# Kernel tuning notes

Measured on AMD Instinct MI355X. Metric: run time of the kernel, lower is better.

Reference implementation:

```python
import jax, jax.numpy as jnp
import numpy as np

EPS = 0.1        # entropic regularization
MAX_ITER = 50    # fixed iteration count (torch early-stops on host; we run all iters)
P = 1            # cost exponent
N_POINTS = 4096
D_FEAT = 2


def _cost_matrix(x, y):
    # x: [N, D], y: [M, D] -> C: [N, M], sum_d |x_i - y_j|^p
    return jnp.sum(jnp.abs(x[:, None, :] - y[None, :, :]) ** P, axis=-1)


def setup_inputs() -> dict:
    key = jax.random.key(0)
    k1, k2 = jax.random.split(key)
    x = jax.random.normal(k1, (N_POINTS, D_FEAT), dtype=jnp.float32)
    y = jax.random.normal(k2, (N_POINTS, D_FEAT), dtype=jnp.float32)
    return {"x": x, "y": y}


def reference(x, y):
    n, m = x.shape[0], y.shape[0]
    C = _cost_matrix(x, y)  # [N, M]
    log_mu = jnp.log(jnp.full((n,), 1.0 / n, dtype=x.dtype) + 1e-8)
    log_nu = jnp.log(jnp.full((m,), 1.0 / m, dtype=y.dtype) + 1e-8)

    def M(u, v):
        # modified cost: (-C + u_i + v_j) / eps
        return (-C + u[:, None] + v[None, :]) / EPS

    def step(carry, _):
        u, v = carry
        u = EPS * (log_mu - jax.scipy.special.logsumexp(M(u, v), axis=-1)) + u
        v = EPS * (log_nu - jax.scipy.special.logsumexp(M(u, v), axis=-2)) + v
        return (u, v), None

    u0 = jnp.zeros((n,), dtype=x.dtype)
    v0 = jnp.zeros((m,), dtype=y.dtype)
    (u, v), _ = jax.lax.scan(step, (u0, v0), None, length=MAX_ITER)

    pi = jnp.exp(M(u, v))                 # transport plan [N, M]
    cost = jnp.sum(pi * C)                # scalar (reduction='none', 2D input)
    return cost ** (1.0 / P), pi, C
```

## Files before the change

### kernel.cpp

```cpp
#include <hip/hip_runtime.h>


#define NPTS    4096
#define EPS_F   0.1f
#define S_L2E   14.426950408889634f
#define INV_SL  0.0693147180559945f
#define A_LOGMU (-0.8317725207f)
#define N_ITER  50
#define NLEAF   16
#define BSTRIDE 64
#define BAR_INTS ((NLEAF + 1 + NLEAF) * BSTRIDE)

typedef float f4u __attribute__((ext_vector_type(4), aligned(4)));

__device__ __forceinline__ float fexp2(float x) {
#if __has_builtin(__builtin_amdgcn_exp2f)
  return __builtin_amdgcn_exp2f(x);
#else
  float r;
  asm("v_exp_f32 %0, %1" : "=v"(r) : "v"(x));
  return r;
#endif
}

__device__ __forceinline__ float coh_load(const float* p) {
  return __hip_atomic_load(p, __ATOMIC_RELAXED, __HIP_MEMORY_SCOPE_AGENT);
}
__device__ __forceinline__ void coh_store(float* p, float x) {
  __hip_atomic_store(p, x, __ATOMIC_RELAXED, __HIP_MEMORY_SCOPE_AGENT);
}

__device__ __forceinline__ float wave_sum64(float x) {
#pragma unroll
  for (int off = 32; off > 0; off >>= 1) x += __shfl_xor(x, off, 64);
  return x;
}

__device__ __forceinline__ void grid_barrier(int* bar, int k, int arrpl) {
  __syncthreads();
  if (threadIdx.x == 0) {
    const int myleaf = blockIdx.x & (NLEAF - 1);
    const int old = __hip_atomic_fetch_add(bar + myleaf * BSTRIDE, 1,
                                           __ATOMIC_RELAXED,
                                           __HIP_MEMORY_SCOPE_AGENT);
    if (old == arrpl * k - 1)
      __hip_atomic_store(bar + (NLEAF + 1 + myleaf) * BSTRIDE, k,
                         __ATOMIC_RELAXED, __HIP_MEMORY_SCOPE_AGENT);
    for (;;) {
      int mn = k;
#pragma unroll
      for (int rr = 0; rr < NLEAF; ++rr) {
        const int f = __hip_atomic_load(bar + (NLEAF + 1 + rr) * BSTRIDE,
                                        __ATOMIC_RELAXED,
                                        __HIP_MEMORY_SCOPE_AGENT);
        mn = min(mn, f);
      }
      if (mn >= k) break;
      __builtin_amdgcn_s_sleep(1);
    }
  }
  __syncthreads();
}

#define QBLK  512
#define QTPB  1024
#define QARR  (QBLK / NLEAF)
#define QC    1024

__device__ __forceinline__ void stageWq(const float* __restrict__ part,
                                        float* __restrict__ sW, int tid,
                                        int colbase, bool zero) {
  float w = 0.f;
  if (!zero) {
    const int g = colbase + tid;
    const float s = ((coh_load(part + g) + coh_load(part + NPTS + g)) +
                     coh_load(part + 2 * NPTS + g)) +
                    coh_load(part + 3 * NPTS + g);
    w = (A_LOGMU - INV_SL * __log2f(s)) * S_L2E;
  }
  sW[tid] = w;
  __syncthreads();
}

__device__ __forceinline__ void phaseq(
    const float rx0, const float ry0, const float rx1, const float ry1,
    const float* __restrict__ sW, const float* __restrict__ sC0,
    const float* __restrict__ sC1, float* __restrict__ pout, int q, int row0,
    int lane) {
  float acc0 = 0.f, acc1 = 0.f;
#pragma unroll
  for (int jt = 0; jt < 4; ++jt) {
    const int j = lane * 4 + jt * 256;
    const float4 W  = *(const float4*)(sW + j);
    const float4 C0 = *(const float4*)(sC0 + j);
    const float4 C1 = *(const float4*)(sC1 + j);
    {
      const float a0 = (W.x - fabsf(rx0 - C0.x)) - fabsf(ry0 - C1.x);
      const float a1 = (W.y - fabsf(rx0 - C0.y)) - fabsf(ry0 - C1.y);
      const float a2 = (W.z - fabsf(rx0 - C0.z)) - fabsf(ry0 - C1.z);
      const float a3 = (W.w - fabsf(rx0 - C0.w)) - fabsf(ry0 - C1.w);
      acc0 += (fexp2(a0) + fexp2(a1)) + (fexp2(a2) + fexp2(a3));
    }
    {
      const float a0 = (W.x - fabsf(rx1 - C0.x)) - fabsf(ry1 - C1.x);
      const float a1 = (W.y - fabsf(rx1 - C0.y)) - fabsf(ry1 - C1.y);
      const float a2 = (W.z - fabsf(rx1 - C0.z)) - fabsf(ry1 - C1.z);
      const float a3 = (W.w - fabsf(rx1 - C0.w)) - fabsf(ry1 - C1.w);
      acc1 += (fexp2(a0) + fexp2(a1)) + (fexp2(a2) + fexp2(a3));
    }
  }
  const float S0 = wave_sum64(acc0);
  const float S1 = wave_sum64(acc1);
  if (lane == 0) {
    coh_store(pout + q * NPTS + row0, S0);
    coh_store(pout + q * NPTS + row0 + 1, S1);
  }
}

__global__ void __launch_bounds__(QTPB, 8)
sinkhorn_quarter(const float* __restrict__ x, const float* __restrict__ y,
                 float* __restrict__ pu, float* __restrict__ pv,
                 float* __restrict__ out, int* __restrict__ bar) {
  __shared__ float sW[QC];
  __shared__ float sC0u[QC], sC1u[QC];
  __shared__ float sC0v[QC], sC1v[QC];
  __shared__ float sCost[16];

  const int tid  = threadIdx.x;
  const int wv   = tid >> 6;
  const int lane = tid & 63;
  const int q    = blockIdx.x & 3;
  const int rg   = blockIdx.x >> 2;
  const int row0 = rg * 32 + wv * 2;
  const int colbase = q * QC;

  float rxu[2], ryu[2], rxv[2], ryv[2];
#pragma unroll
  for (int r = 0; r < 2; ++r) {
    const float2 xr = ((const float2*)x)[row0 + r];
    const float2 yr = ((const float2*)y)[row0 + r];
    rxu[r] = xr.x * S_L2E;  ryu[r] = xr.y * S_L2E;
    rxv[r] = yr.x * S_L2E;  ryv[r] = yr.y * S_L2E;
  }

  {
    const int g = colbase + tid;
    const float2 yc = ((const float2*)y)[g];
    const float2 xc = ((const float2*)x)[g];
    sC0u[tid] = yc.x * S_L2E;  sC1u[tid] = yc.y * S_L2E;
    sC0v[tid] = xc.x * S_L2E;  sC1v[tid] = xc.y * S_L2E;
  }
  __syncthreads();

  int k = 0;
  for (int it = 0; it < N_ITER; ++it) {
    stageWq(pv, sW, tid, colbase, it == 0);
    phaseq(rxu[0], ryu[0], rxu[1], ryu[1], sW, sC0u, sC1u, pu, q, row0, lane);
    grid_barrier(bar, ++k, QARR);
    stageWq(pu, sW, tid, colbase, false);
    phaseq(rxv[0], ryv[0], rxv[1], ryv[1], sW, sC0v, sC1v, pv, q, row0, lane);
    grid_barrier(bar, ++k, QARR);
  }
  stageWq(pv, sW, tid, colbase, false);

  float* __restrict__ pi = out + 1;
  float* __restrict__ cm = out + 1 + (size_t)NPTS * NPTS;
  float uu[2];
#pragma unroll
  for (int r = 0; r < 2; ++r) {
    const int g = row0 + r;
    const float su = ((coh_load(pu + g) + coh_load(pu + NPTS + g)) +
                      coh_load(pu + 2 * NPTS + g)) +
                     coh_load(pu + 3 * NPTS + g);
    uu[r] = (A_LOGMU - INV_SL * __log2f(su)) * S_L2E;
  }

  float costacc = 0.f;
#pragma unroll
  for (int jt = 0; jt < 4; ++jt) {
    const int j = lane * 4 + jt * 256;
    const float4 W  = *(const float4*)(sW + j);
    const float4 C0 = *(const float4*)(sC0u + j);
    const float4 C1 = *(const float4*)(sC1u + j);
#pragma unroll
    for (int r = 0; r < 2; ++r) {
      const float s0 = fabsf(rxu[r] - C0.x) + fabsf(ryu[r] - C1.x);
      const float s1 = fabsf(rxu[r] - C0.y) + fabsf(ryu[r] - C1.y);
      const float s2 = fabsf(rxu[r] - C0.z) + fabsf(ryu[r] - C1.z);
      const float s3 = fabsf(rxu[r] - C0.w) + fabsf(ryu[r] - C1.w);
      const float p0 = fexp2((uu[r] + W.x) - s0);
      const float p1 = fexp2((uu[r] + W.y) - s1);
      const float p2 = fexp2((uu[r] + W.z) - s2);
      const float p3 = fexp2((uu[r] + W.w) - s3);
      costacc = fmaf(p0, s0, costacc);
      costacc = fmaf(p1, s1, costacc);
      costacc = fmaf(p2, s2, costacc);
      costacc = fmaf(p3, s3, costacc);
      const size_t off = (size_t)(row0 + r) * NPTS + colbase + j;
      f4u pvv; pvv.x = p0; pvv.y = p1; pvv.z = p2; pvv.w = p3;
      f4u cv;  cv.x = s0 * INV_SL; cv.y = s1 * INV_SL;
      cv.z = s2 * INV_SL; cv.w = s3 * INV_SL;
      *(f4u*)(pi + off) = pvv;
      *(f4u*)(cm + off) = cv;
    }
  }
  const float cw = wave_sum64(costacc);
  if (lane == 0) sCost[wv] = cw;
  __syncthreads();
  if (tid == 0) {
    float c = 0.f;
#pragma unroll
    for (int w = 0; w < 16; ++w) c += sCost[w];
    atomicAdd(out, c * INV_SL);
  }
}

#define FBLK  256
#define FTPB  1024
#define WPB   (FTPB / 64)
#define RPW   2
#define HALFC 2048
#define NJT   (HALFC / 256)
#define FARR  (FBLK / NLEAF)

__device__ __forceinline__ void fb_stageW(const float* __restrict__ win,
                                          float* __restrict__ sW, int tid) {
  const int c = tid * 4;
  const float w0 = coh_load(win + c + 0), w1 = coh_load(win + c + 1);
  const float w2 = coh_load(win + c + 2), w3 = coh_load(win + c + 3);
  float4 W;
  W.x = w0 * S_L2E;  W.y = w1 * S_L2E;  W.z = w2 * S_L2E;  W.w = w3 * S_L2E;
  *(float4*)(sW + c) = W;
  __syncthreads();
}

__device__ __forceinline__ void fb_stageCoords(const float* __restrict__ colp,
                                               float* __restrict__ sC0,
                                               float* __restrict__ sC1,
                                               int tid) {
  const int c = tid * 4;
  const float4 a = ((const float4*)colp)[(c >> 1) + 0];
  const float4 b = ((const float4*)colp)[(c >> 1) + 1];
  float4 C0, C1;
  C0.x = a.x * S_L2E; C0.y = a.z * S_L2E; C0.z = b.x * S_L2E; C0.w = b.z * S_L2E;
  C1.x = a.y * S_L2E; C1.y = a.w * S_L2E; C1.z = b.y * S_L2E; C1.w = b.w * S_L2E;
  *(float4*)(sC0 + c) = C0;
  *(float4*)(sC1 + c) = C1;
}

__device__ __forceinline__ void fb_phase(const float* __restrict__ rx,
                                         const float* __restrict__ ry,
                                         const float* __restrict__ sW,
                                         const float* __restrict__ sC0,
                                         const float* __restrict__ sC1,
                                         float (*sPart)[RPW],
                                         float* __restrict__ wout,
                                         int row0blk, int wv, int lane,
                                         int tid, int base) {
  float acc0 = 0.f, acc1 = 0.f;
#pragma unroll
  for (int jt = 0; jt < NJT; ++jt) {
    const int j = base + jt * 256;
    const float4 W  = *(const float4*)(sW + j);
    const float4 C0 = *(const float4*)(sC0 + j);
    const float4 C1 = *(const float4*)(sC1 + j);
    {
      const float a0 = (W.x - fabsf(rx[0] - C0.x)) - fabsf(ry[0] - C1.x);
      const float a1 = (W.y - fabsf(rx[0] - C0.y)) - fabsf(ry[0] - C1.y);
      const float a2 = (W.z - fabsf(rx[0] - C0.z)) - fabsf(ry[0] - C1.z);
      const float a3 = (W.w - fabsf(rx[0] - C0.w)) - fabsf(ry[0] - C1.w);
      acc0 += (fexp2(a0) + fexp2(a1)) + (fexp2(a2) + fexp2(a3));
    }
    {
      const float a0 = (W.x - fabsf(rx[1] - C0.x)) - fabsf(ry[1] - C1.x);
      const float a1 = (W.y - fabsf(rx[1] - C0.y)) - fabsf(ry[1] - C1.y);
      const float a2 = (W.z - fabsf(rx[1] - C0.z)) - fabsf(ry[1] - C1.z);
      const float a3 = (W.w - fabsf(rx[1] - C0.w)) - fabsf(ry[1] - C1.w);
      acc1 += (fexp2(a0) + fexp2(a1)) + (fexp2(a2) + fexp2(a3));
    }
  }
  const float S0 = wave_sum64(acc0);
  const float S1 = wave_sum64(acc1);
  if (lane == 0) { sPart[wv][0] = S0; sPart[wv][1] = S1; }
  __syncthreads();
  if (tid < 16) {
    const int p = tid >> 1, r = tid & 1;
    const float S = sPart[2 * p][r] + sPart[2 * p + 1][r];
    coh_store(wout + row0blk + p * RPW + r, A_LOGMU - EPS_F * __logf(S));
  }
}

__global__ void __launch_bounds__(FTPB, 4)
sinkhorn_fallback(const float* __restrict__ x, const float* __restrict__ y,
                  float* __restrict__ u, float* __restrict__ v,
                  float* __restrict__ out, int* __restrict__ bar) {
  __shared__ float sW[NPTS];
  __shared__ float sC0y[NPTS], sC1y[NPTS];
  __shared__ float sC0x[NPTS], sC1x[NPTS];
  __shared__ float sPart[WPB][RPW];
  __shared__ float sCost[WPB];

  const int tid  = threadIdx.x;
  const int wv   = tid >> 6;
  const int lane = tid & 63;
  const int row0blk = blockIdx.x * (WPB / 2) * RPW;
  const int row0 = row0blk + (wv >> 1) * RPW;
  const int base = (wv & 1) * HALFC + lane * 4;

  float rxu[RPW], ryu[RPW], rxv[RPW], ryv[RPW];
#pragma unroll
  for (int r = 0; r < RPW; ++r) {
    const float2 xr = ((const float2*)x)[row0 + r];
    const float2 yr = ((const float2*)y)[row0 + r];
    rxu[r] = xr.x * S_L2E;  ryu[r] = xr.y * S_L2E;
    rxv[r] = yr.x * S_L2E;  ryv[r] = yr.y * S_L2E;
  }

  fb_stageCoords(y, sC0y, sC1y, tid);
  fb_stageCoords(x, sC0x, sC1x, tid);
  __syncthreads();

  int k = 0;
  for (int it = 0; it < N_ITER; ++it) {
    fb_stageW(v, sW, tid);
    fb_phase(rxu, ryu, sW, sC0y, sC1y, sPart, u, row0blk, wv, lane, tid, base);
    grid_barrier(bar, ++k, FARR);
    fb_stageW(u, sW, tid);
    fb_phase(rxv, ryv, sW, sC0x, sC1x, sPart, v, row0blk, wv, lane, tid, base);
    grid_barrier(bar, ++k, FARR);
  }
  fb_stageW(v, sW, tid);

  float* __restrict__ pi = out + 1;
  float* __restrict__ cm = out + 1 + (size_t)NPTS * NPTS;
  float uu[RPW];
#pragma unroll
  for (int r = 0; r < RPW; ++r) uu[r] = coh_load(u + row0 + r) * S_L2E;

  float costacc = 0.f;
#pragma unroll 2
  for (int jt = 0; jt < NJT; ++jt) {
    const int j = base + jt * 256;
    const float4 W  = *(const float4*)(sW + j);
    const float4 C0 = *(const float4*)(sC0y + j);
    const float4 C1 = *(const float4*)(sC1y + j);
#pragma unroll
    for (int r = 0; r < RPW; ++r) {
      const float s0 = fabsf(rxu[r] - C0.x) + fabsf(ryu[r] - C1.x);
      const float s1 = fabsf(rxu[r] - C0.y) + fabsf(ryu[r] - C1.y);
      const float s2 = fabsf(rxu[r] - C0.z) + fabsf(ryu[r] - C1.z);
      const float s3 = fabsf(rxu[r] - C0.w) + fabsf(ryu[r] - C1.w);
      const float p0 = fexp2((uu[r] + W.x) - s0);
      const float p1 = fexp2((uu[r] + W.y) - s1);
      const float p2 = fexp2((uu[r] + W.z) - s2);
      const float p3 = fexp2((uu[r] + W.w) - s3);
      costacc = fmaf(p0, s0, costacc);
      costacc = fmaf(p1, s1, costacc);
      costacc = fmaf(p2, s2, costacc);
      costacc = fmaf(p3, s3, costacc);
      const size_t off = (size_t)(row0 + r) * NPTS + j;
      f4u pvv; pvv.x = p0; pvv.y = p1; pvv.z = p2; pvv.w = p3;
      f4u cv;  cv.x = s0 * INV_SL; cv.y = s1 * INV_SL;
      cv.z = s2 * INV_SL; cv.w = s3 * INV_SL;
      *(f4u*)(pi + off) = pvv;
      *(f4u*)(cm + off) = cv;
    }
  }
  const float cw = wave_sum64(costacc);
  if (lane == 0) sCost[wv] = cw;
  __syncthreads();
  if (tid == 0) {
    float c = 0.f;
#pragma unroll
    for (int w = 0; w < WPB; ++w) c += sCost[w];
    atomicAdd(out, c * INV_SL);
  }
}

__global__ void sinkhorn_init(float* __restrict__ buf, int* __restrict__ bar,
                              float* __restrict__ out) {
  const int i = blockIdx.x * blockDim.x + threadIdx.x;
  if (i < 8 * NPTS) coh_store(buf + i, 0.f);
  if (i < BAR_INTS)
    __hip_atomic_store(bar + i, 0, __ATOMIC_RELAXED, __HIP_MEMORY_SCOPE_AGENT);
  if (i == 0) out[0] = 0.f;
}

extern "C" void kernel_launch(void* const* d_in, const int* in_sizes, int n_in,
                              void* d_out, int out_size, void* d_ws,
                              size_t ws_size, hipStream_t stream) {
  const float* x = (const float*)d_in[0];
  const float* y = (const float*)d_in[1];
  float* pu = (float*)d_ws;
  float* pv = pu + 4 * NPTS;
  int* bar = (int*)(pv + 4 * NPTS);
  float* out = (float*)d_out;

  sinkhorn_init<<<dim3(128), dim3(256), 0, stream>>>(pu, bar, out);

  int maxb = 0;
  hipOccupancyMaxActiveBlocksPerMultiprocessor(&maxb, sinkhorn_quarter, QTPB,
                                               0);

  if (maxb >= 2) {
    void* args[6];
    args[0] = (void*)&x;  args[1] = (void*)&y;
    args[2] = (void*)&pu; args[3] = (void*)&pv;
    args[4] = (void*)&out; args[5] = (void*)&bar;
    hipLaunchCooperativeKernel((void*)sinkhorn_quarter, dim3(QBLK), dim3(QTPB),
                               args, 0, stream);
  } else {
    float* u = pu;
    float* v = pv;
    void* args[6];
    args[0] = (void*)&x;  args[1] = (void*)&y;
    args[2] = (void*)&u;  args[3] = (void*)&v;
    args[4] = (void*)&out; args[5] = (void*)&bar;
    hipLaunchCooperativeKernel((void*)sinkhorn_fallback, dim3(FBLK),
                               dim3(FTPB), args, 0, stream);
  }
}
```

Measured before the change: 716.4 us.

## Replace grid barriers with per-block dependency flags and double-buffered partials

Removes the two full grid barriers per Sinkhorn iteration. Each block now publishes a per-block completion flag and waits only on the 128 producer blocks whose partial sums feed its column quarter. The u/v partial-sum buffers are double-buffered by iteration parity, so fast blocks can run ahead without overwriting data that slower blocks still need. This trades a global sync for many more flag polls per block (128 threads spinning), which adds memory traffic to the flag lines.

Measured after the change: 708.5 us. No clear change (-1.1%).

```diff
diff --git a/kernel.cpp b/kernel.cpp
--- a/kernel.cpp
+++ b/kernel.cpp
@@ -29,6 +29,12 @@
 __device__ __forceinline__ void coh_store(float* p, float x) {
   __hip_atomic_store(p, x, __ATOMIC_RELAXED, __HIP_MEMORY_SCOPE_AGENT);
 }
+__device__ __forceinline__ int coh_load_i(const int* p) {
+  return __hip_atomic_load(p, __ATOMIC_RELAXED, __HIP_MEMORY_SCOPE_AGENT);
+}
+__device__ __forceinline__ void coh_store_i(int* p, int x) {
+  __hip_atomic_store(p, x, __ATOMIC_RELAXED, __HIP_MEMORY_SCOPE_AGENT);
+}
 
 __device__ __forceinline__ float wave_sum64(float x) {
 #pragma unroll
@@ -36,50 +42,20 @@
   return x;
 }
 
-__device__ __forceinline__ void grid_barrier(int* bar, int k, int arrpl) {
-  __syncthreads();
-  if (threadIdx.x == 0) {
-    const int myleaf = blockIdx.x & (NLEAF - 1);
-    const int old = __hip_atomic_fetch_add(bar + myleaf * BSTRIDE, 1,
-                                           __ATOMIC_RELAXED,
-                                           __HIP_MEMORY_SCOPE_AGENT);
-    if (old == arrpl * k - 1)
-      __hip_atomic_store(bar + (NLEAF + 1 + myleaf) * BSTRIDE, k,
-                         __ATOMIC_RELAXED, __HIP_MEMORY_SCOPE_AGENT);
-    for (;;) {
-      int mn = k;
-#pragma unroll
-      for (int rr = 0; rr < NLEAF; ++rr) {
-        const int f = __hip_atomic_load(bar + (NLEAF + 1 + rr) * BSTRIDE,
-                                        __ATOMIC_RELAXED,
-                                        __HIP_MEMORY_SCOPE_AGENT);
-        mn = min(mn, f);
-      }
-      if (mn >= k) break;
-      __builtin_amdgcn_s_sleep(1);
-    }
-  }
-  __syncthreads();
-}
-
 #define QBLK  512
 #define QTPB  1024
-#define QARR  (QBLK / NLEAF)
 #define QC    1024
-
-__device__ __forceinline__ void stageWq(const float* __restrict__ part,
-                                        float* __restrict__ sW, int tid,
-                                        int colbase, bool zero) {
-  float w = 0.f;
-  if (!zero) {
-    const int g = colbase + tid;
-    const float s = ((coh_load(part + g) + coh_load(part + NPTS + g)) +
-                     coh_load(part + 2 * NPTS + g)) +
-                    coh_load(part + 3 * NPTS + g);
-    w = (A_LOGMU - INV_SL * __log2f(s)) * S_L2E;
-  }
-  sW[tid] = w;
-  __syncthreads();
+#define FSTR  32
+#define PLANE (4 * NPTS)
+
+__device__ __forceinline__ void stage_from(const float* __restrict__ P,
+                                           float* __restrict__ sW, int tid,
+                                           int colbase) {
+  const int g = colbase + tid;
+  const float s = ((coh_load(P + g) + coh_load(P + NPTS + g)) +
+                   coh_load(P + 2 * NPTS + g)) +
+                  coh_load(P + 3 * NPTS + g);
+  sW[tid] = (A_LOGMU - INV_SL * __log2f(s)) * S_L2E;
 }
 
 __device__ __forceinline__ void phaseq(
@@ -118,9 +94,10 @@
 }
 
 __global__ void __launch_bounds__(QTPB, 8)
-sinkhorn_quarter(const float* __restrict__ x, const float* __restrict__ y,
-                 float* __restrict__ pu, float* __restrict__ pv,
-                 float* __restrict__ out, int* __restrict__ bar) {
+sinkhorn_flags(const float* __restrict__ x, const float* __restrict__ y,
+               float* __restrict__ pu, float* __restrict__ pv,
+               int* __restrict__ uflg, int* __restrict__ vflg,
+               float* __restrict__ out) {
   __shared__ float sW[QC];
   __shared__ float sC0u[QC], sC1u[QC];
   __shared__ float sC0v[QC], sC1v[QC];
@@ -133,6 +110,8 @@
   const int rg   = blockIdx.x >> 2;
   const int row0 = rg * 32 + wv * 2;
   const int colbase = q * QC;
+  const int b = blockIdx.x;
+  const int pbase = q * 128;
 
   float rxu[2], ryu[2], rxv[2], ryv[2];
 #pragma unroll
@@ -142,7 +121,6 @@
     rxu[r] = xr.x * S_L2E;  ryu[r] = xr.y * S_L2E;
     rxv[r] = yr.x * S_L2E;  ryv[r] = yr.y * S_L2E;
   }
-
   {
     const int g = colbase + tid;
     const float2 yc = ((const float2*)y)[g];
@@ -152,26 +130,53 @@
   }
   __syncthreads();
 
-  int k = 0;
   for (int it = 0; it < N_ITER; ++it) {
-    stageWq(pv, sW, tid, colbase, it == 0);
-    phaseq(rxu[0], ryu[0], rxu[1], ryu[1], sW, sC0u, sC1u, pu, q, row0, lane);
-    grid_barrier(bar, ++k, QARR);
-    stageWq(pu, sW, tid, colbase, false);
-    phaseq(rxv[0], ryv[0], rxv[1], ryv[1], sW, sC0v, sC1v, pv, q, row0, lane);
-    grid_barrier(bar, ++k, QARR);
-  }
-  stageWq(pv, sW, tid, colbase, false);
+    if (it > 0 && tid < 128)
+      while (coh_load_i(vflg + (pbase + tid) * FSTR) < it)
+        __builtin_amdgcn_s_sleep(1);
+    __syncthreads();
+    if (it > 0)
+      stage_from(pv + ((it - 1) & 1) * PLANE, sW, tid, colbase);
+    else
+      sW[tid] = 0.f;
+    __syncthreads();
+    phaseq(rxu[0], ryu[0], rxu[1], ryu[1], sW, sC0u, sC1u,
+           pu + (it & 1) * PLANE, q, row0, lane);
+    __syncthreads();
+    if (tid == 0) coh_store_i(uflg + b * FSTR, it + 1);
+
+    if (tid < 128)
+      while (coh_load_i(uflg + (pbase + tid) * FSTR) < it + 1)
+        __builtin_amdgcn_s_sleep(1);
+    __syncthreads();
+    stage_from(pu + (it & 1) * PLANE, sW, tid, colbase);
+    __syncthreads();
+    phaseq(rxv[0], ryv[0], rxv[1], ryv[1], sW, sC0v, sC1v,
+           pv + (it & 1) * PLANE, q, row0, lane);
+    __syncthreads();
+    if (tid == 0) coh_store_i(vflg + b * FSTR, it + 1);
+  }
+
+  if (tid < 128)
+    while (coh_load_i(vflg + (pbase + tid) * FSTR) < N_ITER)
+      __builtin_amdgcn_s_sleep(1);
+  else if (tid < 132)
+    while (coh_load_i(uflg + (rg * 4 + (tid - 128)) * FSTR) < N_ITER)
+      __builtin_amdgcn_s_sleep(1);
+  __syncthreads();
+  stage_from(pv + ((N_ITER - 1) & 1) * PLANE, sW, tid, colbase);
+  __syncthreads();
 
   float* __restrict__ pi = out + 1;
   float* __restrict__ cm = out + 1 + (size_t)NPTS * NPTS;
+  const float* __restrict__ PU = pu + ((N_ITER - 1) & 1) * PLANE;
   float uu[2];
 #pragma unroll
   for (int r = 0; r < 2; ++r) {
     const int g = row0 + r;
-    const float su = ((coh_load(pu + g) + coh_load(pu + NPTS + g)) +
-                      coh_load(pu + 2 * NPTS + g)) +
-                     coh_load(pu + 3 * NPTS + g);
+    const float su = ((coh_load(PU + g) + coh_load(PU + NPTS + g)) +
+                      coh_load(PU + 2 * NPTS + g)) +
+                     coh_load(PU + 3 * NPTS + g);
     uu[r] = (A_LOGMU - INV_SL * __log2f(su)) * S_L2E;
   }
 
@@ -223,6 +228,32 @@
 #define NJT   (HALFC / 256)
 #define FARR  (FBLK / NLEAF)
 
+__device__ __forceinline__ void grid_barrier(int* bar, int k, int arrpl) {
+  __syncthreads();
+  if (threadIdx.x == 0) {
+    const int myleaf = blockIdx.x & (NLEAF - 1);
+    const int old = __hip_atomic_fetch_add(bar + myleaf * BSTRIDE, 1,
+                                           __ATOMIC_RELAXED,
+                                           __HIP_MEMORY_SCOPE_AGENT);
+    if (old == arrpl * k - 1)
+      __hip_atomic_store(bar + (NLEAF + 1 + myleaf) * BSTRIDE, k,
+                         __ATOMIC_RELAXED, __HIP_MEMORY_SCOPE_AGENT);
+    for (;;) {
+      int mn = k;
+#pragma unroll
+      for (int rr = 0; rr < NLEAF; ++rr) {
+        const int f = __hip_atomic_load(bar + (NLEAF + 1 + rr) * BSTRIDE,
+                                        __ATOMIC_RELAXED,
+                                        __HIP_MEMORY_SCOPE_AGENT);
+        mn = min(mn, f);
+      }
+      if (mn >= k) break;
+      __builtin_amdgcn_s_sleep(1);
+    }
+  }
+  __syncthreads();
+}
+
 __device__ __forceinline__ void fb_stageW(const float* __restrict__ win,
                                           float* __restrict__ sW, int tid) {
   const int c = tid * 4;
@@ -377,10 +408,17 @@
   }
 }
 
-__global__ void sinkhorn_init(float* __restrict__ buf, int* __restrict__ bar,
+#define NFLG (QBLK * FSTR)
+
+__global__ void sinkhorn_init(float* __restrict__ planes,
+                              int* __restrict__ flags,
+                              int* __restrict__ bar,
                               float* __restrict__ out) {
   const int i = blockIdx.x * blockDim.x + threadIdx.x;
-  if (i < 8 * NPTS) coh_store(buf + i, 0.f);
+  if (i < 4 * PLANE) coh_store(planes + i, 0.f);
+  if (i < 2 * NFLG)
+    __hip_atomic_store(flags + i, 0, __ATOMIC_RELAXED,
+                       __HIP_MEMORY_SCOPE_AGENT);
   if (i < BAR_INTS)
     __hip_atomic_store(bar + i, 0, __ATOMIC_RELAXED, __HIP_MEMORY_SCOPE_AGENT);
   if (i == 0) out[0] = 0.f;
@@ -392,26 +430,28 @@
   const float* x = (const float*)d_in[0];
   const float* y = (const float*)d_in[1];
   float* pu = (float*)d_ws;
-  float* pv = pu + 4 * NPTS;
-  int* bar = (int*)(pv + 4 * NPTS);
+  float* pv = pu + 2 * PLANE;
+  int* uflg = (int*)(pv + 2 * PLANE);
+  int* vflg = uflg + NFLG;
+  int* bar  = vflg + NFLG;
   float* out = (float*)d_out;
 
-  sinkhorn_init<<<dim3(128), dim3(256), 0, stream>>>(pu, bar, out);
+  sinkhorn_init<<<dim3(256), dim3(256), 0, stream>>>(pu, uflg, bar, out);
 
   int maxb = 0;
-  hipOccupancyMaxActiveBlocksPerMultiprocessor(&maxb, sinkhorn_quarter, QTPB,
-                                               0);
+  hipOccupancyMaxActiveBlocksPerMultiprocessor(&maxb, sinkhorn_flags, QTPB, 0);
 
   if (maxb >= 2) {
-    void* args[6];
-    args[0] = (void*)&x;  args[1] = (void*)&y;
-    args[2] = (void*)&pu; args[3] = (void*)&pv;
-    args[4] = (void*)&out; args[5] = (void*)&bar;
-    hipLaunchCooperativeKernel((void*)sinkhorn_quarter, dim3(QBLK), dim3(QTPB),
+    void* args[7];
+    args[0] = (void*)&x;    args[1] = (void*)&y;
+    args[2] = (void*)&pu;   args[3] = (void*)&pv;
+    args[4] = (void*)&uflg; args[5] = (void*)&vflg;
+    args[6] = (void*)&out;
+    hipLaunchCooperativeKernel((void*)sinkhorn_flags, dim3(QBLK), dim3(QTPB),
                                args, 0, stream);
   } else {
     float* u = pu;
-    float* v = pv;
+    float* v = pu + NPTS;
     void* args[6];
     args[0] = (void*)&x;  args[1] = (void*)&y;
     args[2] = (void*)&u;  args[3] = (void*)&v;
```
